# Optimization experiments

Hardware: AMD Instinct MI355X
Metric: run time of the kernel (lower is better)

The kernel has to match this reference:

```python
import jax, jax.numpy as jnp
import numpy as np

RC = 5.0                 # cutoff radius (init kwarg)
B, M = 128, 256          # structures per batch, atoms per structure
L = 17.2                 # box edge (Angstrom) -> ~0.05 atoms/A^3, ~27 nbrs/atom at rc=5
P = 2_097_152            # fixed max pair count (output padding)


def _pairs(coord):
    """Cell-list candidate generation + radius filter, batched over structures.

    Faithful to the TF CellListNL (no 'cell' / open-boundary path): atoms are
    shifted to the positive octant, binned into cells of edge rc, and candidate
    pairs are atoms of the same structure whose cell bins differ by at most 1 in
    every dimension (the 27-cell stencil). Final pairs satisfy 0 < dist < rc.
    """
    pos = coord - jnp.min(coord, axis=0)                          # [N,3] shift (as in TF code)
    cell = jnp.floor(pos / RC).astype(jnp.int32)                  # [N,3] cell bins
    posb = pos.reshape(B, M, 3)
    cellb = cell.reshape(B, M, 3)
    diff = posb[:, None, :, :] - posb[:, :, None, :]              # [B,M,M,3] = pos_j - pos_i
    sq = jnp.sum(diff * diff, axis=-1)                            # [B,M,M]
    nz = sq > 0.0
    dist = jnp.sqrt(jnp.where(nz, sq, 1.0)) * nz                  # safe norm (0 on diagonal)
    # 27-neighbor-cell stencil == per-axis bin difference in {-1,0,1}
    nbr = jnp.all(jnp.abs(cellb[:, None, :, :] - cellb[:, :, None, :]) <= 1, axis=-1)
    mask = nbr & (dist < RC) & nz                                 # [B,M,M]
    return diff, dist, mask


def setup_inputs() -> dict:
    key = jax.random.key(0)
    coord = jax.random.uniform(key, (B * M, 3), jnp.float32) * L  # atoms in [0,L)^3 per structure
    ind_1 = jnp.repeat(jnp.arange(B, dtype=jnp.int32), M)         # structure index per atom
    return {"coord": coord, "ind_1": ind_1}


def reference(coord, ind_1):
    # ind_1 is encoded structurally: atoms are laid out as B contiguous blocks of M,
    # so same-structure pairing is enforced by the batched [B,M,M] computation.
    diff, dist, mask = _pairs(coord)
    b, i, j = jnp.nonzero(mask, size=P, fill_value=0)             # fixed-size pair list
    valid = mask[b, i, j]                                         # False on padded rows
    d = dist[b, i, j] * valid                                     # [P]
    df = diff[b, i, j] * valid[:, None]                           # [P,3]
    ind_2 = jnp.stack([b * M + i, b * M + j], axis=1) * valid[:, None].astype(jnp.int32)
    return ind_2, d, df
```

## Files before the change

kernel.cpp:

```cpp
#include <hip/hip_runtime.h>
#include <float.h>

#define MM 256
#define PP 2097152
#define NBLK 512
#define CBLK 256
#define GTH (NBLK * 256)
#define CAP 2048
#define SQMAX 24.999996185302734375f

typedef unsigned long long u64;


__device__ inline void wave_min3(float& x, float& y, float& z) {
    #pragma unroll
    for (int off = 32; off > 0; off >>= 1) {
        x = fminf(x, __shfl_xor(x, off, 64));
        y = fminf(y, __shfl_xor(y, off, 64));
        z = fminf(z, __shfl_xor(z, off, 64));
    }
}

__device__ inline void zero_range(float* __restrict__ o, int lo, int hi, int g) {
    int a = (lo + 3) & ~3;
    if (a > hi) a = hi;
    if (g < a - lo) o[lo + g] = 0.0f;
    float4* o4 = reinterpret_cast<float4*>(o);
    const float4 z4 = make_float4(0.f, 0.f, 0.f, 0.f);
    for (int q = (a >> 2) + g; q < (hi >> 2); q += GTH) o4[q] = z4;
}

__device__ inline void flush_plane(const float* __restrict__ lds, int n, int pad,
                                   float* __restrict__ gdst, int t) {
    if (n <= 0) return;
    const int end = pad + n;
    const int nb = (end + 3) >> 2;
    for (int m = t; m < nb; m += 256) {
        const int lo = m << 2;
        if (lo >= pad && lo + 4 <= end) {
            *reinterpret_cast<float4*>(gdst + lo) =
                *reinterpret_cast<const float4*>(lds + lo);
        } else {
            const int a = lo < pad ? pad : lo;
            const int bmax = (lo + 4 < end) ? (lo + 4) : end;
            for (int e = a; e < bmax; ++e) gdst[e] = lds[e];
        }
    }
}


__global__ void __launch_bounds__(512)
count_k(const float* __restrict__ coord, float* __restrict__ minvec,
        u64* __restrict__ masks, int* __restrict__ bsums) {
    const int cb = blockIdx.x;
    const int b = cb >> 1, h = cb & 1;
    const int t = threadIdx.x;
    const int lane = t & 63, w = t >> 6;

    __shared__ float4 tile4[4][65];
    __shared__ float lmin[3][8];
    __shared__ int wsum[8];

    const float4* c4 = reinterpret_cast<const float4*>(coord);
    float mx = FLT_MAX, my = FLT_MAX, mz = FLT_MAX;
    int r = t % 3;
    #pragma unroll 6
    for (int k = 0; k < 48; ++k) {
        const float4 f = c4[k * 512 + t];
        const float p = fminf(f.x, f.w);
        const float vx = (r == 0) ? p : ((r == 1) ? f.z : f.y);
        const float vy = (r == 1) ? p : ((r == 0) ? f.y : f.z);
        const float vz = (r == 2) ? p : ((r == 0) ? f.z : f.y);
        mx = fminf(mx, vx);
        my = fminf(my, vy);
        mz = fminf(mz, vz);
        r += 2; if (r >= 3) r -= 3;
    }
    wave_min3(mx, my, mz);
    if (lane == 0) { lmin[0][w] = mx; lmin[1][w] = my; lmin[2][w] = mz; }
    __syncthreads();
    mx = fminf(fminf(fminf(lmin[0][0], lmin[0][1]), fminf(lmin[0][2], lmin[0][3])),
               fminf(fminf(lmin[0][4], lmin[0][5]), fminf(lmin[0][6], lmin[0][7])));
    my = fminf(fminf(fminf(lmin[1][0], lmin[1][1]), fminf(lmin[1][2], lmin[1][3])),
               fminf(fminf(lmin[1][4], lmin[1][5]), fminf(lmin[1][6], lmin[1][7])));
    mz = fminf(fminf(fminf(lmin[2][0], lmin[2][1]), fminf(lmin[2][2], lmin[2][3])),
               fminf(fminf(lmin[2][4], lmin[2][5]), fminf(lmin[2][6], lmin[2][7])));
    if (cb == 0 && t == 0) { minvec[0] = mx; minvec[1] = my; minvec[2] = mz; }

    if (t < 256) {
        const int ja = b * MM + t;
        tile4[t >> 6][t & 63] = make_float4(__fsub_rn(coord[3 * ja + 0], mx),
                                            __fsub_rn(coord[3 * ja + 1], my),
                                            __fsub_rn(coord[3 * ja + 2], mz), 0.0f);
    }
    __syncthreads();

    const int rblk = 2 * h + (t >> 8);
    const int tt = t & 255;
    const int i_loc = tt >> 2, c = tt & 3;
    const float4 pi4 = tile4[rblk][i_loc];
    u64 m = 0ULL;
    for (int jj = 0; jj < 64; ++jj) {
        float4 v = tile4[c][jj];
        float dx = __fsub_rn(v.x, pi4.x);
        float dy = __fsub_rn(v.y, pi4.y);
        float dz = __fsub_rn(v.z, pi4.z);
        float sq = __fadd_rn(__fadd_rn(__fmul_rn(dx, dx), __fmul_rn(dy, dy)),
                             __fmul_rn(dz, dz));
        if (sq > 0.0f && sq <= SQMAX) m |= (1ULL << jj);
    }
    masks[cb * 512 + t] = m;

    int v = __popcll(m);
    #pragma unroll
    for (int off = 32; off > 0; off >>= 1) v += __shfl_xor(v, off, 64);
    if (lane == 0) wsum[w] = v;
    __syncthreads();
    if (t == 0) {
        bsums[cb * 2 + 0] = wsum[0] + wsum[1] + wsum[2] + wsum[3];
        bsums[cb * 2 + 1] = wsum[4] + wsum[5] + wsum[6] + wsum[7];
    }
}

__global__ void __launch_bounds__(256)
write_k(const float* __restrict__ coord, const float* __restrict__ minvec,
        const u64* __restrict__ masks, const int* __restrict__ bsums,
        float* __restrict__ outF) {
    const int b2 = blockIdx.x;
    const int b = b2 >> 2, rblk = b2 & 3;
    const int t = threadIdx.x;
    const int lane = t & 63, w = t >> 6;

    __shared__ float4 tile4[4][65];
    __shared__ int pre[NBLK];
    __shared__ int sTot;
    __shared__ int wsum[4];
    __shared__ __align__(16) float sd[CAP + 4];
    __shared__ __align__(16) float sind[2 * CAP + 4];
    __shared__ __align__(16) float sdf[3 * CAP + 4];

    const u64 mask = masks[b2 * 256 + t];
    const float mnx = minvec[0], mny = minvec[1], mnz = minvec[2];
    const int ja = b * MM + t;
    tile4[w][lane] = make_float4(__fsub_rn(coord[3 * ja + 0], mnx),
                                 __fsub_rn(coord[3 * ja + 1], mny),
                                 __fsub_rn(coord[3 * ja + 2], mnz), 0.0f);

    if (w == 0) {
        int v[8]; int s = 0;
        #pragma unroll
        for (int q = 0; q < 8; ++q) { v[q] = bsums[lane * 8 + q]; s += v[q]; }
        int isum = s;
        #pragma unroll
        for (int off = 1; off < 64; off <<= 1) {
            int u = __shfl_up(isum, off, 64);
            if (lane >= off) isum += u;
        }
        int run = isum - s;
        #pragma unroll
        for (int q = 0; q < 8; ++q) { pre[lane * 8 + q] = run; run += v[q]; }
        if (lane == 63) sTot = run;
    }
    __syncthreads();
    const int base = pre[b2];
    const int total = (sTot < PP) ? sTot : PP;

    const int cnt = __popcll(mask);
    int incl = cnt;
    #pragma unroll
    for (int off = 1; off < 64; off <<= 1) {
        int v = __shfl_up(incl, off, 64);
        if (lane >= off) incl += v;
    }
    if (lane == 63) wsum[w] = incl;
    __syncthreads();
    const int agg = wsum[0] + wsum[1] + wsum[2] + wsum[3];
    int woff = 0;
    for (int k = 0; k < w; ++k) woff += wsum[k];
    const int lexcl = woff + incl - cnt;

    const int i_loc = t >> 2, c = t & 3;
    const float4 pi4 = tile4[rblk][i_loc];
    const int gi = b * MM + rblk * 64 + i_loc;
    const int gj0 = b * MM + c * 64;

    const int nbat = (agg + CAP - 1) / CAP;
    for (int bb = 0; bb < nbat; ++bb) {
        const int wlo = bb * CAP, whi = wlo + CAP;
        const int pbase = base + wlo;
        const int pd = pbase & 3;
        const int pi = (2 * pbase) & 3;
        const int pf = (3 * pbase) & 3;
        int q = lexcl;
        u64 mm = mask;
        while (mm) {
            const int jj = __ffsll((long long)mm) - 1;
            mm &= mm - 1;
            if (q >= whi) break;
            if (q >= wlo) {
                float4 v = tile4[c][jj];
                float dx = __fsub_rn(v.x, pi4.x);
                float dy = __fsub_rn(v.y, pi4.y);
                float dz = __fsub_rn(v.z, pi4.z);
                float sq = __fadd_rn(__fadd_rn(__fmul_rn(dx, dx), __fmul_rn(dy, dy)),
                                     __fmul_rn(dz, dz));
                const int s = q - wlo;
                sd[s + pd] = __fsqrt_rn(sq);
                sind[2 * s + pi + 0] = (float)gi;
                sind[2 * s + pi + 1] = (float)(gj0 + jj);
                sdf[3 * s + pf + 0] = dx;
                sdf[3 * s + pf + 1] = dy;
                sdf[3 * s + pf + 2] = dz;
            }
            q++;
        }
        __syncthreads();
        const int nq = ((agg - wlo) < CAP) ? (agg - wlo) : CAP;
        int rem = PP - pbase; if (rem < 0) rem = 0;
        const int nv = (nq < rem) ? nq : rem;
        flush_plane(sd,   nv,     pd, outF + 2 * PP + pbase - pd,     t);
        flush_plane(sind, 2 * nv, pi, outF + 2 * pbase - pi,          t);
        flush_plane(sdf,  3 * nv, pf, outF + 3 * PP + 3 * pbase - pf, t);
        __syncthreads();
    }

    const int g = b2 * 256 + t;
    zero_range(outF, 2 * total,          2 * PP, g);
    zero_range(outF, 2 * PP + total,     3 * PP, g);
    zero_range(outF, 3 * PP + 3 * total, 6 * PP, g);
}

extern "C" void kernel_launch(void* const* d_in, const int* in_sizes, int n_in,
                              void* d_out, int out_size, void* d_ws, size_t ws_size,
                              hipStream_t stream) {
    const float* coord = (const float*)d_in[0];
    float* outF = (float*)d_out;

    u64*   masks  = (u64*)d_ws;
    int*   bsums  = (int*)(masks + GTH);
    float* minvec = (float*)(bsums + NBLK);

    count_k<<<CBLK, 512, 0, stream>>>(coord, minvec, masks, bsums);
    write_k<<<NBLK, 256, 0, stream>>>(coord, minvec, masks, bsums, outF);
}
```

Measured before the change: 28.90 us.

## Replace LDS-staged per-thread pair emission with per-pair binary-search scatter

The write kernel no longer walks each thread's bitmask serially into LDS staging buffers and then flushes them with vector stores. Instead it builds a prefix table of per-thread offsets, and each thread handles output pairs k, t, t+256 and so on. For each pair it binary-searches the owning mask, finds the r-th set bit by clearing bits, recomputes the geometry and writes directly to global memory. This balances work across lanes and removes the staging passes and barriers, at the cost of uncoalesced 3-float scattered writes and a bit-clear loop per pair. The count loop also gets an unroll-by-8 hint.

```diff
diff --git a/kernel.cpp b/kernel.cpp
--- a/kernel.cpp
+++ b/kernel.cpp
@@ -6,7 +6,6 @@
 #define NBLK 512
 #define CBLK 256
 #define GTH (NBLK * 256)
-#define CAP 2048
 #define SQMAX 24.999996185302734375f
 
 typedef unsigned long long u64;
@@ -28,24 +27,6 @@
     float4* o4 = reinterpret_cast<float4*>(o);
     const float4 z4 = make_float4(0.f, 0.f, 0.f, 0.f);
     for (int q = (a >> 2) + g; q < (hi >> 2); q += GTH) o4[q] = z4;
-}
-
-__device__ inline void flush_plane(const float* __restrict__ lds, int n, int pad,
-                                   float* __restrict__ gdst, int t) {
-    if (n <= 0) return;
-    const int end = pad + n;
-    const int nb = (end + 3) >> 2;
-    for (int m = t; m < nb; m += 256) {
-        const int lo = m << 2;
-        if (lo >= pad && lo + 4 <= end) {
-            *reinterpret_cast<float4*>(gdst + lo) =
-                *reinterpret_cast<const float4*>(lds + lo);
-        } else {
-            const int a = lo < pad ? pad : lo;
-            const int bmax = (lo + 4 < end) ? (lo + 4) : end;
-            for (int e = a; e < bmax; ++e) gdst[e] = lds[e];
-        }
-    }
 }
 
 
@@ -100,6 +81,7 @@
     const int i_loc = tt >> 2, c = tt & 3;
     const float4 pi4 = tile4[rblk][i_loc];
     u64 m = 0ULL;
+    #pragma unroll 8
     for (int jj = 0; jj < 64; ++jj) {
         float4 v = tile4[c][jj];
         float dx = __fsub_rn(v.x, pi4.x);
@@ -135,11 +117,11 @@
     __shared__ int pre[NBLK];
     __shared__ int sTot;
     __shared__ int wsum[4];
-    __shared__ __align__(16) float sd[CAP + 4];
-    __shared__ __align__(16) float sind[2 * CAP + 4];
-    __shared__ __align__(16) float sdf[3 * CAP + 4];
+    __shared__ u64 smask[256];
+    __shared__ int thrOff[257];
 
     const u64 mask = masks[b2 * 256 + t];
+    smask[t] = mask;
     const float mnx = minvec[0], mny = minvec[1], mnz = minvec[2];
     const int ja = b * MM + t;
     tile4[w][lane] = make_float4(__fsub_rn(coord[3 * ja + 0], mnx),
@@ -161,9 +143,6 @@
         for (int q = 0; q < 8; ++q) { pre[lane * 8 + q] = run; run += v[q]; }
         if (lane == 63) sTot = run;
     }
-    __syncthreads();
-    const int base = pre[b2];
-    const int total = (sTot < PP) ? sTot : PP;
 
     const int cnt = __popcll(mask);
     int incl = cnt;
@@ -174,54 +153,47 @@
     }
     if (lane == 63) wsum[w] = incl;
     __syncthreads();
-    const int agg = wsum[0] + wsum[1] + wsum[2] + wsum[3];
     int woff = 0;
     for (int k = 0; k < w; ++k) woff += wsum[k];
-    const int lexcl = woff + incl - cnt;
-
-    const int i_loc = t >> 2, c = t & 3;
-    const float4 pi4 = tile4[rblk][i_loc];
-    const int gi = b * MM + rblk * 64 + i_loc;
-    const int gj0 = b * MM + c * 64;
-
-    const int nbat = (agg + CAP - 1) / CAP;
-    for (int bb = 0; bb < nbat; ++bb) {
-        const int wlo = bb * CAP, whi = wlo + CAP;
-        const int pbase = base + wlo;
-        const int pd = pbase & 3;
-        const int pi = (2 * pbase) & 3;
-        const int pf = (3 * pbase) & 3;
-        int q = lexcl;
-        u64 mm = mask;
-        while (mm) {
-            const int jj = __ffsll((long long)mm) - 1;
-            mm &= mm - 1;
-            if (q >= whi) break;
-            if (q >= wlo) {
-                float4 v = tile4[c][jj];
-                float dx = __fsub_rn(v.x, pi4.x);
-                float dy = __fsub_rn(v.y, pi4.y);
-                float dz = __fsub_rn(v.z, pi4.z);
-                float sq = __fadd_rn(__fadd_rn(__fmul_rn(dx, dx), __fmul_rn(dy, dy)),
-                                     __fmul_rn(dz, dz));
-                const int s = q - wlo;
-                sd[s + pd] = __fsqrt_rn(sq);
-                sind[2 * s + pi + 0] = (float)gi;
-                sind[2 * s + pi + 1] = (float)(gj0 + jj);
-                sdf[3 * s + pf + 0] = dx;
-                sdf[3 * s + pf + 1] = dy;
-                sdf[3 * s + pf + 2] = dz;
-            }
-            q++;
+    thrOff[t] = woff + incl - cnt;
+    if (t == 255) thrOff[256] = woff + incl;
+    __syncthreads();
+
+    const int base = pre[b2];
+    const int agg = thrOff[256];
+    const int total = (sTot < PP) ? sTot : PP;
+
+    for (int k = t; k < agg; k += 256) {
+        const int p = base + k;
+        if (p >= PP) break;
+        int lo = 0, hi = 256;
+        #pragma unroll
+        for (int s = 0; s < 8; ++s) {
+            const int mid = (lo + hi) >> 1;
+            if (thrOff[mid] <= k) lo = mid; else hi = mid;
         }
-        __syncthreads();
-        const int nq = ((agg - wlo) < CAP) ? (agg - wlo) : CAP;
-        int rem = PP - pbase; if (rem < 0) rem = 0;
-        const int nv = (nq < rem) ? nq : rem;
-        flush_plane(sd,   nv,     pd, outF + 2 * PP + pbase - pd,     t);
-        flush_plane(sind, 2 * nv, pi, outF + 2 * pbase - pi,          t);
-        flush_plane(sdf,  3 * nv, pf, outF + 3 * PP + 3 * pbase - pf, t);
-        __syncthreads();
+        const int u = lo;
+        int r = k - thrOff[u];
+        u64 mm = smask[u];
+        while (r--) mm &= mm - 1;
+        const int jj = __ffsll((long long)mm) - 1;
+
+        const int iu = u >> 2, cu = u & 3;
+        const float4 pi4 = tile4[rblk][iu];
+        const float4 v = tile4[cu][jj];
+        const float dx = __fsub_rn(v.x, pi4.x);
+        const float dy = __fsub_rn(v.y, pi4.y);
+        const float dz = __fsub_rn(v.z, pi4.z);
+        const float sq = __fadd_rn(__fadd_rn(__fmul_rn(dx, dx), __fmul_rn(dy, dy)),
+                                   __fmul_rn(dz, dz));
+        outF[2 * PP + p] = __fsqrt_rn(sq);
+        float2 ind2 = make_float2((float)(b * MM + rblk * 64 + iu),
+                                  (float)(b * MM + cu * 64 + jj));
+        *reinterpret_cast<float2*>(outF + 2 * p) = ind2;
+        const int dfb = 3 * PP + 3 * p;
+        outF[dfb + 0] = dx;
+        outF[dfb + 1] = dy;
+        outF[dfb + 2] = dz;
     }
 
     const int g = b2 * 256 + t;
```

New measurement: 28.96 us. No clear change (+0.2%).
